# Performance work log

Measured on AMD Instinct MI355X. Metric: run time of the kernel, lower is better.

Reference implementation:

```python
import jax, jax.numpy as jnp
import numpy as np

B, H, W, C = 32, 56, 56, 512
NH, WS, SS = 16, 7, 3
HD = C // NH
N = WS * WS
HID = int(C * 4.0)
SCALE = HD ** -0.5
EPS = 1e-5


def _window_partition(x):
    # x: (B, H, W, C) -> (B*nW, WS, WS, C)
    b = x.shape[0]
    x = x.reshape(b, H // WS, WS, W // WS, WS, C)
    return x.transpose(0, 1, 3, 2, 4, 5).reshape(-1, WS, WS, C)


def _window_reverse(wins):
    b = wins.shape[0] // ((H // WS) * (W // WS))
    x = wins.reshape(b, H // WS, W // WS, WS, WS, C)
    return x.transpose(0, 1, 3, 2, 4, 5).reshape(b, H, W, C)


def _ln(x, g, b):
    mu = jnp.mean(x, -1, keepdims=True)
    var = jnp.mean((x - mu) ** 2, -1, keepdims=True)
    return (x - mu) * jax.lax.rsqrt(var + EPS) * g + b


def setup_inputs():
    key = jax.random.key(0)
    ks = jax.random.split(key, 8)

    def w(k, shape, s=0.02):
        return jax.random.normal(k, shape, jnp.float32) * s

    # relative position index (static, same recipe as Swin)
    coords = np.stack(np.meshgrid(np.arange(WS), np.arange(WS), indexing='ij'))  # (2,WS,WS)
    cf = coords.reshape(2, -1)
    rel = (cf[:, :, None] - cf[:, None, :]).transpose(1, 2, 0).astype(np.int64)
    rel[:, :, 0] += WS - 1
    rel[:, :, 1] += WS - 1
    rel[:, :, 0] *= 2 * WS - 1
    rel_index = jnp.asarray(rel.sum(-1), jnp.int32)  # (N, N)

    # shifted-window attention mask (static)
    img = np.zeros((H, W), np.float32)
    cnt = 0
    for hs in (slice(0, -WS), slice(-WS, -SS), slice(-SS, None)):
        for vs in (slice(0, -WS), slice(-WS, -SS), slice(-SS, None)):
            img[hs, vs] = cnt
            cnt += 1
    mw = img.reshape(H // WS, WS, W // WS, WS).transpose(0, 2, 1, 3).reshape(-1, N)
    am = mw[:, None, :] - mw[:, :, None]
    attn_mask = jnp.asarray(np.where(am != 0, -100.0, 0.0).astype(np.float32))  # (nW, N, N)

    return {
        'x': jax.random.normal(ks[0], (B, H * W, C), jnp.float32),
        'norm1_g': jnp.ones((C,), jnp.float32), 'norm1_b': jnp.zeros((C,), jnp.float32),
        'qkv_w': w(ks[1], (C, 3 * C)), 'qkv_b': jnp.zeros((3 * C,), jnp.float32),
        'rel_bias_table': w(ks[2], ((2 * WS - 1) ** 2, NH)),
        'proj_w': w(ks[3], (C, C)), 'proj_b': jnp.zeros((C,), jnp.float32),
        'norm2_g': jnp.ones((C,), jnp.float32), 'norm2_b': jnp.zeros((C,), jnp.float32),
        'fc1_w': w(ks[4], (C, HID)), 'fc1_b': jnp.zeros((HID,), jnp.float32),
        'fc2_w': w(ks[5], (HID, C)), 'fc2_b': jnp.zeros((C,), jnp.float32),
        'rel_index': rel_index,
        'attn_mask': attn_mask,
    }


def reference(x, norm1_g, norm1_b, qkv_w, qkv_b, rel_bias_table, proj_w, proj_b,
              norm2_g, norm2_b, fc1_w, fc1_b, fc2_w, fc2_b, rel_index, attn_mask):
    shortcut = x
    h = _ln(x, norm1_g, norm1_b).reshape(B, H, W, C)
    # cyclic shift (shift_size > 0 -> SW-MSA)
    h = jnp.roll(h, shift=(-SS, -SS), axis=(1, 2))
    wins = _window_partition(h).reshape(-1, N, C)  # (B*nW, N, C)
    Bn = wins.shape[0]

    qkv = (wins @ qkv_w + qkv_b).reshape(Bn, N, 3, NH, HD).transpose(2, 0, 3, 1, 4)
    q, k, v = qkv[0] * SCALE, qkv[1], qkv[2]  # (Bn, NH, N, HD)
    attn = jnp.einsum('bhnd,bhmd->bhnm', q, k)  # (Bn, NH, N, N)

    bias = rel_bias_table[rel_index.reshape(-1)].reshape(N, N, NH).transpose(2, 0, 1)
    attn = attn + bias[None]

    nW = attn_mask.shape[0]
    attn = attn.reshape(Bn // nW, nW, NH, N, N) + attn_mask[None, :, None]
    attn = jax.nn.softmax(attn.reshape(Bn, NH, N, N), axis=-1)

    o = jnp.einsum('bhnm,bhmd->bhnd', attn, v).transpose(0, 2, 1, 3).reshape(Bn, N, C)
    o = o @ proj_w + proj_b

    h = _window_reverse(o.reshape(-1, WS, WS, C))
    h = jnp.roll(h, shift=(SS, SS), axis=(1, 2)).reshape(B, H * W, C)
    x = shortcut + h

    m = _ln(x, norm2_g, norm2_b)
    m = jax.nn.gelu(m @ fc1_w + fc1_b, approximate=False) @ fc2_w + fc2_b
    return x + m
```

## Files before the change

kernel.cpp:

```cpp
#include <hip/hip_runtime.h>
#include <hip/hip_bf16.h>


typedef unsigned short u16;
typedef __bf16 bf16x8 __attribute__((ext_vector_type(8)));
typedef float floatx4 __attribute__((ext_vector_type(4)));

#define MROWS 100352
#define SCALE_ATTN 0.17677669529663687f

__device__ __forceinline__ float b2f(u16 u) {
    union { unsigned int i; float f; } c; c.i = ((unsigned int)u) << 16; return c.f;
}
__device__ __forceinline__ u16 f2b(float f) {
    union { float f; unsigned int u; } c; c.f = f;
    unsigned int r = c.u + 0x7fffu + ((c.u >> 16) & 1u);
    return (u16)(r >> 16);
}

__device__ __forceinline__ int win_token(int win, int n) {
    int b  = win >> 6;
    int wi = (win & 63) >> 3;
    int wj = win & 7;
    int ti = n / 7;
    int tj = n - ti * 7;
    int ii = wi * 7 + ti + 3; if (ii >= 56) ii -= 56;
    int jj = wj * 7 + tj + 3; if (jj >= 56) jj -= 56;
    return b * 3136 + ii * 56 + jj;
}

__global__ void detect_flag(const unsigned int* __restrict__ g1, int* __restrict__ flag) {
    if (threadIdx.x == 0 && blockIdx.x == 0)
        *flag = (g1[0] == 0x3F800000u) ? 1 : 0;
}

__global__ __launch_bounds__(256)
void conv_f32(const void* __restrict__ src, float* __restrict__ dst, int n,
              const int* __restrict__ flag) {
    int i = blockIdx.x * 256 + threadIdx.x;
    if (i >= n) return;
    if (*flag) dst[i] = ((const float*)src)[i];
    else       dst[i] = b2f(((const u16*)src)[i]);
}

__global__ __launch_bounds__(256)
void transpose_k(const void* __restrict__ srcv, u16* __restrict__ dst, int R, int Cc,
                 const int* __restrict__ flag) {
    const bool f32 = (*flag != 0);
    __shared__ u16 tile[32][33];
    int tx = threadIdx.x & 31, ty = threadIdx.x >> 5;
    int c0 = blockIdx.x << 5, r0 = blockIdx.y << 5;
#pragma unroll
    for (int j = 0; j < 4; ++j) {
        size_t idx = (size_t)(r0 + ty + j * 8) * Cc + c0 + tx;
        tile[ty + j * 8][tx] = f32 ? f2b(((const float*)srcv)[idx]) : ((const u16*)srcv)[idx];
    }
    __syncthreads();
#pragma unroll
    for (int j = 0; j < 4; ++j)
        dst[(size_t)(c0 + ty + j * 8) * R + r0 + tx] = tile[tx][ty + j * 8];
}

__global__ __launch_bounds__(256)
void bias_expand(const float* __restrict__ tblf, const int* __restrict__ ridx,
                 float* __restrict__ biasf) {
    int i = blockIdx.x * 256 + threadIdx.x;
    if (i < 16 * 2401) {
        int head = i / 2401, r = i - head * 2401;
        biasf[i] = tblf[ridx[r] * 16 + head];
    }
}

template <bool REMAP>
__global__ __launch_bounds__(256)
void ln_kernel(const void* __restrict__ srcv, const float* __restrict__ g,
               const float* __restrict__ bb, u16* __restrict__ dst,
               const int* __restrict__ flag) {
    int row = blockIdx.x;
    size_t srow;
    if (REMAP) {
        int win = row / 49, n = row - win * 49;
        srow = (size_t)win_token(win, n);
    } else {
        srow = (size_t)row;
    }
    int t = threadIdx.x;
    float v0, v1;
    if (REMAP && *flag) {
        float2 u = *(const float2*)((const float*)srcv + srow * 512 + t * 2);
        v0 = u.x; v1 = u.y;
    } else {
        ushort2 u = *(const ushort2*)((const u16*)srcv + srow * 512 + t * 2);
        v0 = b2f(u.x); v1 = b2f(u.y);
    }
    float sum = v0 + v1, sq = v0 * v0 + v1 * v1;
#pragma unroll
    for (int off = 32; off > 0; off >>= 1) {
        sum += __shfl_down(sum, off);
        sq  += __shfl_down(sq, off);
    }
    __shared__ float s1[4], s2[4];
    int wv = t >> 6, ln = t & 63;
    if (ln == 0) { s1[wv] = sum; s2[wv] = sq; }
    __syncthreads();
    float tot  = s1[0] + s1[1] + s1[2] + s1[3];
    float tot2 = s2[0] + s2[1] + s2[2] + s2[3];
    float mean = tot * (1.0f / 512.0f);
    float var  = tot2 * (1.0f / 512.0f) - mean * mean;
    float rstd = rsqrtf(var + 1e-5f);
    float o0 = (v0 - mean) * rstd * g[t * 2]     + bb[t * 2];
    float o1 = (v1 - mean) * rstd * g[t * 2 + 1] + bb[t * 2 + 1];
    ushort2 ou; ou.x = f2b(o0); ou.y = f2b(o1);
    *(ushort2*)(dst + (size_t)row * 512 + t * 2) = ou;
}

template <int MODE>
__global__ __launch_bounds__(256)
void gemm128(const u16* __restrict__ A, const u16* __restrict__ Bt,
             const float* __restrict__ bias, int K, int Nn,
             void* __restrict__ outv, const void* __restrict__ resv,
             const int* __restrict__ flag, int row_off) {
    __shared__ __align__(16) u16 As[128 * 32];
    __shared__ __align__(16) u16 Bs[128 * 32];
    const int tid = threadIdx.x;
    const int bm = blockIdx.x, bn = blockIdx.y;
    const int wave = tid >> 6, lane = tid & 63;
    const int wr = (wave >> 1) << 6, wc = (wave & 1) << 6;
    const int lm = lane & 15, lq = lane >> 4;

    floatx4 acc[4][4];
#pragma unroll
    for (int i = 0; i < 4; ++i)
#pragma unroll
        for (int j = 0; j < 4; ++j)
            acc[i][j] = (floatx4){0.f, 0.f, 0.f, 0.f};

    const size_t arow0 = (size_t)bm * 128;
    const size_t brow0 = (size_t)bn * 128;

    const int c0 = wave << 1;
    const int rA = (c0 << 4) + (lane >> 2);
    const int kc = (lane & 3) << 3;
    const u16* gA0 = A  + (arow0 + rA) * K + kc;
    const u16* gA1 = gA0 + (size_t)16 * K;
    const u16* gB0 = Bt + (brow0 + rA) * K + kc;
    const u16* gB1 = gB0 + (size_t)16 * K;
    u16* lA0 = As + (c0 << 9);
    u16* lA1 = lA0 + 512;
    u16* lB0 = Bs + (c0 << 9);
    u16* lB1 = lB0 + 512;

    for (int k0 = 0; k0 < K; k0 += 32) {
        __builtin_amdgcn_global_load_lds(
            (const __attribute__((address_space(1))) void*)(gA0 + k0),
            (__attribute__((address_space(3))) void*)lA0, 16, 0, 0);
        __builtin_amdgcn_global_load_lds(
            (const __attribute__((address_space(1))) void*)(gA1 + k0),
            (__attribute__((address_space(3))) void*)lA1, 16, 0, 0);
        __builtin_amdgcn_global_load_lds(
            (const __attribute__((address_space(1))) void*)(gB0 + k0),
            (__attribute__((address_space(3))) void*)lB0, 16, 0, 0);
        __builtin_amdgcn_global_load_lds(
            (const __attribute__((address_space(1))) void*)(gB1 + k0),
            (__attribute__((address_space(3))) void*)lB1, 16, 0, 0);
        __syncthreads();
        bf16x8 af[4], bf[4];
#pragma unroll
        for (int i = 0; i < 4; ++i)
            af[i] = *(const bf16x8*)(&As[(wr + (i << 4) + lm) * 32 + (lq << 3)]);
#pragma unroll
        for (int j = 0; j < 4; ++j)
            bf[j] = *(const bf16x8*)(&Bs[(wc + (j << 4) + lm) * 32 + (lq << 3)]);
#pragma unroll
        for (int i = 0; i < 4; ++i)
#pragma unroll
            for (int j = 0; j < 4; ++j)
                acc[i][j] = __builtin_amdgcn_mfma_f32_16x16x32_bf16(af[i], bf[j], acc[i][j], 0, 0, 0);
        __syncthreads();
    }

    const bool f32 = (MODE >= 2) ? (*flag != 0) : false;
#pragma unroll
    for (int i = 0; i < 4; ++i) {
#pragma unroll
        for (int r = 0; r < 4; ++r) {
            const int row = (bm << 7) + wr + (i << 4) + (lq << 2) + r;
            size_t orow;
            if (MODE == 2) {
                int win = row / 49, n = row - win * 49;
                orow = (size_t)win_token(win, n);
            } else {
                orow = (size_t)row;
            }
#pragma unroll
            for (int j = 0; j < 4; ++j) {
                const int col = (bn << 7) + wc + (j << 4) + lm;
                float v = acc[i][j][r] + bias[col];
                if (MODE == 0) {
                    ((u16*)outv)[(size_t)row * Nn + col] = f2b(v);
                } else if (MODE == 1) {
                    v = 0.5f * v * (1.0f + erff(v * 0.70710678118654752f));
                    ((u16*)outv)[(size_t)row * Nn + col] = f2b(v);
                } else if (MODE == 2) {
                    float res = f32 ? ((const float*)resv)[orow * 512 + col]
                                    : b2f(((const u16*)resv)[orow * 512 + col]);
                    ((u16*)outv)[orow * 512 + col] = f2b(v + res);
                } else {
                    float res = b2f(((const u16*)resv)[(size_t)row * Nn + col]);
                    size_t grow = (size_t)(row + row_off);
                    if (f32) ((float*)outv)[grow * Nn + col] = v + res;
                    else     ((u16*)outv)[grow * Nn + col]  = f2b(v + res);
                }
            }
        }
    }
}

__global__ __launch_bounds__(64)
void attn_kernel(const u16* __restrict__ qkv, const float* __restrict__ biasf,
                 const float* __restrict__ amaskf, u16* __restrict__ o, int win_base) {
    const int blk = blockIdx.x;
    const int winl = blk >> 4, head = blk & 15;
    const int wing = win_base + winl;
    const int w = wing & 63;
    const int t = threadIdx.x;
    __shared__ float qf[49 * 32], kf[49 * 32], vf[49 * 32];
    const size_t base = (size_t)winl * 49 * 1536 + head * 32;
    for (int idx = t; idx < 392; idx += 64) {
        int m = idx >> 3, d = (idx & 7) << 2;
        size_t rb = base + (size_t)m * 1536 + d;
        ushort4 uq = *(const ushort4*)(qkv + rb);
        ushort4 uk = *(const ushort4*)(qkv + rb + 512);
        ushort4 uv = *(const ushort4*)(qkv + rb + 1024);
        int o4 = m * 32 + d;
        qf[o4 + 0] = b2f(uq.x); qf[o4 + 1] = b2f(uq.y);
        qf[o4 + 2] = b2f(uq.z); qf[o4 + 3] = b2f(uq.w);
        kf[o4 + 0] = b2f(uk.x); kf[o4 + 1] = b2f(uk.y);
        kf[o4 + 2] = b2f(uk.z); kf[o4 + 3] = b2f(uk.w);
        vf[o4 + 0] = b2f(uv.x); vf[o4 + 1] = b2f(uv.y);
        vf[o4 + 2] = b2f(uv.z); vf[o4 + 3] = b2f(uv.w);
    }
    __syncthreads();
    if (t < 49) {
        float q[32];
#pragma unroll
        for (int d = 0; d < 32; ++d) q[d] = qf[t * 32 + d] * SCALE_ATTN;
        float s[49];
        float mx = -1e30f;
        const float* bp = biasf + head * 2401 + t * 49;
        const float* mp = amaskf + w * 2401 + t * 49;
#pragma unroll
        for (int m = 0; m < 49; ++m) {
            float acc = 0.f;
#pragma unroll
            for (int d = 0; d < 32; ++d) acc += q[d] * kf[m * 32 + d];
            acc += bp[m] + mp[m];
            s[m] = acc;
            mx = fmaxf(mx, acc);
        }
        float sum = 0.f;
#pragma unroll
        for (int m = 0; m < 49; ++m) { s[m] = __expf(s[m] - mx); sum += s[m]; }
        float inv = 1.0f / sum;
        float ov[32];
#pragma unroll
        for (int d = 0; d < 32; ++d) ov[d] = 0.f;
#pragma unroll
        for (int m = 0; m < 49; ++m) {
            float p = s[m];
#pragma unroll
            for (int d = 0; d < 32; ++d) ov[d] += p * vf[m * 32 + d];
        }
        u16* op = o + (size_t)(wing * 49 + t) * 512 + head * 32;
#pragma unroll
        for (int dc = 0; dc < 32; dc += 4) {
            ushort4 pk;
            pk.x = f2b(ov[dc + 0] * inv); pk.y = f2b(ov[dc + 1] * inv);
            pk.z = f2b(ov[dc + 2] * inv); pk.w = f2b(ov[dc + 3] * inv);
            *(ushort4*)(op + dc) = pk;
        }
    }
}

extern "C" void kernel_launch(void* const* d_in, const int* in_sizes, int n_in,
                              void* d_out, int out_size, void* d_ws, size_t ws_size,
                              hipStream_t stream) {
    const void* x      = d_in[0];
    const void* n1g    = d_in[1];
    const void* n1b    = d_in[2];
    const void* qkv_w  = d_in[3];
    const void* qkv_b  = d_in[4];
    const void* relt   = d_in[5];
    const void* proj_w = d_in[6];
    const void* proj_b = d_in[7];
    const void* n2g    = d_in[8];
    const void* n2b    = d_in[9];
    const void* fc1_w  = d_in[10];
    const void* fc1_b  = d_in[11];
    const void* fc2_w  = d_in[12];
    const void* fc2_b  = d_in[13];
    const int*  ridx   = (const int*)d_in[14];
    const void* amask  = d_in[15];

    char* ws = (char*)d_ws;
    u16*  wT_qkv  = (u16*)(ws);
    u16*  wT_proj = (u16*)(ws + 1572864);
    u16*  wT_fc1  = (u16*)(ws + 2097152);
    u16*  wT_fc2  = (u16*)(ws + 4194304);
    float* biasf  = (float*)(ws + 6291456);
    float* amaskf = (float*)(ws + 6445120);
    float* qkv_bf = (float*)(ws + 7059776);
    float* proj_bf= (float*)(ws + 7065920);
    float* fc1_bf = (float*)(ws + 7067968);
    float* fc2_bf = (float*)(ws + 7076160);
    float* n1gf   = (float*)(ws + 7078208);
    float* n1bf   = (float*)(ws + 7080256);
    float* n2gf   = (float*)(ws + 7082304);
    float* n2bf   = (float*)(ws + 7084352);
    float* reltf  = (float*)(ws + 7086400);
    int*   flag   = (int*)(ws + 7097216);
    u16* bufA = (u16*)(ws + 8388608);
    u16* bufB = (u16*)(ws + 8388608 + 102760448);
    u16* bufC = (u16*)(ws + 8388608 + 102760448 + 77070336);

    detect_flag<<<1, 64, 0, stream>>>((const unsigned int*)n1g, flag);

    conv_f32<<<6, 256, 0, stream>>>(qkv_b, qkv_bf, 1536, flag);
    conv_f32<<<2, 256, 0, stream>>>(proj_b, proj_bf, 512, flag);
    conv_f32<<<8, 256, 0, stream>>>(fc1_b, fc1_bf, 2048, flag);
    conv_f32<<<2, 256, 0, stream>>>(fc2_b, fc2_bf, 512, flag);
    conv_f32<<<2, 256, 0, stream>>>(n1g, n1gf, 512, flag);
    conv_f32<<<2, 256, 0, stream>>>(n1b, n1bf, 512, flag);
    conv_f32<<<2, 256, 0, stream>>>(n2g, n2gf, 512, flag);
    conv_f32<<<2, 256, 0, stream>>>(n2b, n2bf, 512, flag);
    conv_f32<<<11, 256, 0, stream>>>(relt, reltf, 169 * 16, flag);
    conv_f32<<<(64 * 2401 + 255) / 256, 256, 0, stream>>>(amask, amaskf, 64 * 2401, flag);

    transpose_k<<<dim3(48, 16), 256, 0, stream>>>(qkv_w, wT_qkv, 512, 1536, flag);
    transpose_k<<<dim3(16, 16), 256, 0, stream>>>(proj_w, wT_proj, 512, 512, flag);
    transpose_k<<<dim3(64, 16), 256, 0, stream>>>(fc1_w, wT_fc1, 512, 2048, flag);
    transpose_k<<<dim3(16, 64), 256, 0, stream>>>(fc2_w, wT_fc2, 2048, 512, flag);
    bias_expand<<<(16 * 2401 + 255) / 256, 256, 0, stream>>>(reltf, ridx, biasf);

    ln_kernel<true><<<MROWS, 256, 0, stream>>>(x, n1gf, n1bf, bufA, flag);

    for (int c = 0; c < 4; ++c) {
        const u16* Ain = bufA + (size_t)c * 25088 * 512;
        gemm128<0><<<dim3(196, 12), 256, 0, stream>>>(Ain, wT_qkv, qkv_bf, 512, 1536, bufB, nullptr, flag, 0);
        attn_kernel<<<512 * 16, 64, 0, stream>>>(bufB, biasf, amaskf, bufC, c * 512);
    }

    gemm128<2><<<dim3(784, 4), 256, 0, stream>>>(bufC, wT_proj, proj_bf, 512, 512, bufA, x, flag, 0);

    ln_kernel<false><<<MROWS, 256, 0, stream>>>(bufA, n2gf, n2bf, bufC, flag);

    for (int mc0 = 0; mc0 < MROWS; mc0 += 16384) {
        int rows = (MROWS - mc0 < 16384) ? (MROWS - mc0) : 16384;
        int tiles = rows >> 7;
        gemm128<1><<<dim3(tiles, 16), 256, 0, stream>>>(bufC + (size_t)mc0 * 512, wT_fc1, fc1_bf, 512, 2048, bufB, nullptr, flag, 0);
        gemm128<3><<<dim3(tiles, 4), 256, 0, stream>>>(bufB, wT_fc2, fc2_bf, 2048, 512, d_out, bufA + (size_t)mc0 * 512, flag, mc0);
    }
}
```

Measured before the change: 2.423 ms.

## Double-buffer GEMM LDS tiles and remap workgroups by XCD for L2 locality

The GEMM kernel now keeps two LDS buffers, issuing the global-to-LDS loads for the next K slice before computing on the current one, with one barrier per iteration instead of two. The launch grid becomes 1D and the block index is remapped so consecutive tiles land on the same XCD, with N-tiles adjacent for a shared A row block, to improve L2 reuse. LDS use doubles, which may lower occupancy. Overlap relies on the async global_load_lds completing before the trailing barrier.

Result: faster. 2.328 ms (-3.9%).

```diff
diff --git a/kernel.cpp b/kernel.cpp
--- a/kernel.cpp
+++ b/kernel.cpp
@@ -28,6 +28,10 @@
     int jj = wj * 7 + tj + 3; if (jj >= 56) jj -= 56;
     return b * 3136 + ii * 56 + jj;
 }
+
+#define GL2LDS(gaddr, laddr) \
+    __builtin_amdgcn_global_load_lds((const __attribute__((address_space(1))) void*)(gaddr), \
+                                     (__attribute__((address_space(3))) void*)(laddr), 16, 0, 0)
 
 __global__ void detect_flag(const unsigned int* __restrict__ g1, int* __restrict__ flag) {
     if (threadIdx.x == 0 && blockIdx.x == 0)
@@ -117,13 +121,22 @@
 template <int MODE>
 __global__ __launch_bounds__(256)
 void gemm128(const u16* __restrict__ A, const u16* __restrict__ Bt,
-             const float* __restrict__ bias, int K, int Nn,
+             const float* __restrict__ bias, int K, int Nn, int nbn,
              void* __restrict__ outv, const void* __restrict__ resv,
              const int* __restrict__ flag, int row_off) {
-    __shared__ __align__(16) u16 As[128 * 32];
-    __shared__ __align__(16) u16 Bs[128 * 32];
+    __shared__ __align__(16) u16 As[2 * 128 * 32];
+    __shared__ __align__(16) u16 Bs[2 * 128 * 32];
     const int tid = threadIdx.x;
-    const int bm = blockIdx.x, bn = blockIdx.y;
+
+    const int nwg = (int)gridDim.x;
+    const int bid = (int)blockIdx.x;
+    const int q = nwg >> 3, r = nwg & 7;
+    const int xcd = bid & 7, idx = bid >> 3;
+    const int base = (xcd < r) ? xcd * (q + 1) : r * (q + 1) + (xcd - r) * q;
+    const int wg = base + idx;
+    const int bm = wg / nbn;
+    const int bn = wg - bm * nbn;
+
     const int wave = tid >> 6, lane = tid & 63;
     const int wr = (wave >> 1) << 6, wc = (wave & 1) << 6;
     const int lm = lane & 15, lq = lane >> 4;
@@ -145,46 +158,44 @@
     const u16* gA1 = gA0 + (size_t)16 * K;
     const u16* gB0 = Bt + (brow0 + rA) * K + kc;
     const u16* gB1 = gB0 + (size_t)16 * K;
-    u16* lA0 = As + (c0 << 9);
-    u16* lA1 = lA0 + 512;
-    u16* lB0 = Bs + (c0 << 9);
-    u16* lB1 = lB0 + 512;
-
+    const int lofs = c0 << 9;
+
+    GL2LDS(gA0, As + lofs); GL2LDS(gA1, As + lofs + 512);
+    GL2LDS(gB0, Bs + lofs); GL2LDS(gB1, Bs + lofs + 512);
+    __syncthreads();
+
+    int cur = 0;
     for (int k0 = 0; k0 < K; k0 += 32) {
-        __builtin_amdgcn_global_load_lds(
-            (const __attribute__((address_space(1))) void*)(gA0 + k0),
-            (__attribute__((address_space(3))) void*)lA0, 16, 0, 0);
-        __builtin_amdgcn_global_load_lds(
-            (const __attribute__((address_space(1))) void*)(gA1 + k0),
-            (__attribute__((address_space(3))) void*)lA1, 16, 0, 0);
-        __builtin_amdgcn_global_load_lds(
-            (const __attribute__((address_space(1))) void*)(gB0 + k0),
-            (__attribute__((address_space(3))) void*)lB0, 16, 0, 0);
-        __builtin_amdgcn_global_load_lds(
-            (const __attribute__((address_space(1))) void*)(gB1 + k0),
-            (__attribute__((address_space(3))) void*)lB1, 16, 0, 0);
-        __syncthreads();
+        const int kn = k0 + 32;
+        if (kn < K) {
+            const int nb = ((cur ^ 1) << 12) + lofs;
+            GL2LDS(gA0 + kn, As + nb); GL2LDS(gA1 + kn, As + nb + 512);
+            GL2LDS(gB0 + kn, Bs + nb); GL2LDS(gB1 + kn, Bs + nb + 512);
+        }
+        const u16* Ab = As + (cur << 12);
+        const u16* Bb = Bs + (cur << 12);
         bf16x8 af[4], bf[4];
 #pragma unroll
         for (int i = 0; i < 4; ++i)
-            af[i] = *(const bf16x8*)(&As[(wr + (i << 4) + lm) * 32 + (lq << 3)]);
+            af[i] = *(const bf16x8*)(&Ab[(wr + (i << 4) + lm) * 32 + (lq << 3)]);
 #pragma unroll
         for (int j = 0; j < 4; ++j)
-            bf[j] = *(const bf16x8*)(&Bs[(wc + (j << 4) + lm) * 32 + (lq << 3)]);
+            bf[j] = *(const bf16x8*)(&Bb[(wc + (j << 4) + lm) * 32 + (lq << 3)]);
 #pragma unroll
         for (int i = 0; i < 4; ++i)
 #pragma unroll
             for (int j = 0; j < 4; ++j)
                 acc[i][j] = __builtin_amdgcn_mfma_f32_16x16x32_bf16(af[i], bf[j], acc[i][j], 0, 0, 0);
         __syncthreads();
+        cur ^= 1;
     }
 
     const bool f32 = (MODE >= 2) ? (*flag != 0) : false;
 #pragma unroll
     for (int i = 0; i < 4; ++i) {
 #pragma unroll
-        for (int r = 0; r < 4; ++r) {
-            const int row = (bm << 7) + wr + (i << 4) + (lq << 2) + r;
+        for (int rr = 0; rr < 4; ++rr) {
+            const int row = (bm << 7) + wr + (i << 4) + (lq << 2) + rr;
             size_t orow;
             if (MODE == 2) {
                 int win = row / 49, n = row - win * 49;
@@ -195,7 +206,7 @@
 #pragma unroll
             for (int j = 0; j < 4; ++j) {
                 const int col = (bn << 7) + wc + (j << 4) + lm;
-                float v = acc[i][j][r] + bias[col];
+                float v = acc[i][j][rr] + bias[col];
                 if (MODE == 0) {
                     ((u16*)outv)[(size_t)row * Nn + col] = f2b(v);
                 } else if (MODE == 1) {
@@ -346,18 +357,18 @@
 
     for (int c = 0; c < 4; ++c) {
         const u16* Ain = bufA + (size_t)c * 25088 * 512;
-        gemm128<0><<<dim3(196, 12), 256, 0, stream>>>(Ain, wT_qkv, qkv_bf, 512, 1536, bufB, nullptr, flag, 0);
+        gemm128<0><<<196 * 12, 256, 0, stream>>>(Ain, wT_qkv, qkv_bf, 512, 1536, 12, bufB, nullptr, flag, 0);
         attn_kernel<<<512 * 16, 64, 0, stream>>>(bufB, biasf, amaskf, bufC, c * 512);
     }
 
-    gemm128<2><<<dim3(784, 4), 256, 0, stream>>>(bufC, wT_proj, proj_bf, 512, 512, bufA, x, flag, 0);
+    gemm128<2><<<784 * 4, 256, 0, stream>>>(bufC, wT_proj, proj_bf, 512, 512, 4, bufA, x, flag, 0);
 
     ln_kernel<false><<<MROWS, 256, 0, stream>>>(bufA, n2gf, n2bf, bufC, flag);
 
     for (int mc0 = 0; mc0 < MROWS; mc0 += 16384) {
         int rows = (MROWS - mc0 < 16384) ? (MROWS - mc0) : 16384;
         int tiles = rows >> 7;
-        gemm128<1><<<dim3(tiles, 16), 256, 0, stream>>>(bufC + (size_t)mc0 * 512, wT_fc1, fc1_bf, 512, 2048, bufB, nullptr, flag, 0);
-        gemm128<3><<<dim3(tiles, 4), 256, 0, stream>>>(bufB, wT_fc2, fc2_bf, 2048, 512, d_out, bufA + (size_t)mc0 * 512, flag, mc0);
-    }
-}
+        gemm128<1><<<tiles * 16, 256, 0, stream>>>(bufC + (size_t)mc0 * 512, wT_fc1, fc1_bf, 512, 2048, 16, bufB, nullptr, flag, 0);
+        gemm128<3><<<tiles * 4, 256, 0, stream>>>(bufB, wT_fc2, fc2_bf, 2048, 512, 4, d_out, bufA + (size_t)mc0 * 512, flag, mc0);
+    }
+}
```
